# Optimization experiments

Hardware: AMD Instinct MI355X
Metric: run time of the kernel (lower is better)

Reference implementation:

```python
import jax, jax.numpy as jnp
import numpy as np

N, D, M, K = 65536, 128, 8, 256


def _quantize_stage(res, C):
    """Nearest-codeword lookup for one residual-quantizer stage.
    res: (N, D) residual vectors; C: (K, D) codebook.
    Returns (recon (N, D), one-hot code (N, K)).
    """
    # squared L2 distances via expansion: ||r||^2 - 2 r.C^T + ||c||^2
    d2 = (jnp.sum(res * res, axis=-1, keepdims=True)
          - 2.0 * jnp.einsum('nd,kd->nk', res, C)
          + jnp.sum(C * C, axis=-1))                      # (N, K)
    idx = jnp.argmin(d2, axis=-1)                          # (N,)
    onehot = jax.nn.one_hot(idx, K, dtype=res.dtype)       # (N, K)
    recon = jnp.einsum('nk,kd->nd', onehot, C)             # gather via one-hot matmul
    return recon, onehot


def setup_inputs() -> dict:
    key = jax.random.key(0)
    kx, kc = jax.random.split(key)
    x = jax.random.normal(kx, (N, D), dtype=jnp.float32)
    # learned codebooks: one (K, D) table per stage, kaiming-uniform-like scale
    bound = float(np.sqrt(6.0 / D))
    codebooks = jax.random.uniform(kc, (M, K, D), dtype=jnp.float32,
                                   minval=-bound, maxval=bound)
    return {"x": x, "codebooks": codebooks}


def reference(x, codebooks):
    # Sequential residual quantization: M stages, strict data dependency.
    x_recon, code0 = _quantize_stage(x, codebooks[0])
    codes = [code0[:, None, :]]          # (N, 1, K)
    side_output = [x_recon]
    res = x - x_recon
    for i in range(1, M):
        res_recon, code = _quantize_stage(res, codebooks[i])
        codes.append(code[:, None, :])
        x_recon = x_recon + res_recon
        side_output.append(x_recon)
        res = x - x_recon
    codes = jnp.concatenate(codes, axis=1)       # (N, M, K) one-hot
    side_output = jnp.stack(side_output, axis=0)  # (M, N, D)
    return (x_recon, codes, side_output)
```

## Files before the change

### kernel.cpp

```cpp
#include <hip/hip_runtime.h>


constexpr int NV = 65536;
constexpr int DD = 128;
constexpr int MS = 8;
constexpr int KC = 256;
constexpr int CH = 112;
constexpr int CST = 20;
constexpr int RST = 8 * CST;

template<int CTRL>
__device__ __forceinline__ float bfly_add(float v) {
    int p = __builtin_amdgcn_update_dpp(__float_as_int(v), __float_as_int(v),
                                        CTRL, 0xF, 0xF, true);
    return v + __int_as_float(p);
}

__global__ __launch_bounds__(256, 2)
void rq_kernel(const float* __restrict__ x,
               const float* __restrict__ cb,
               float* __restrict__ out)
{
    const int tid = threadIdx.x;
    const int c   = tid & 7;
    const int grp = tid >> 3;
    const size_t vbase = (size_t)blockIdx.x * 128 + (size_t)grp * 4;

    __shared__ __align__(16) float sC[CH * RST];
    __shared__ float cn_s[CH];

    float rA[4][16], cA[4][16];

    #pragma unroll
    for (int v = 0; v < 4; ++v) {
        const float* xr = x + (vbase + v) * DD + c;
        #pragma unroll
        for (int k = 0; k < 16; ++k) {
            rA[v][k] = xr[8 * k];
            cA[v][k] = 0.0f;
        }
    }

    float* out_recon = out;
    float* out_codes = out + (size_t)NV * DD;
    float* out_side  = out_codes + (size_t)NV * MS * KC;

    for (int m = 0; m < MS; ++m) {
        const float* C = cb + (size_t)m * KC * DD;

        float rn[4];
        #pragma unroll
        for (int v = 0; v < 4; ++v) {
            float p = rA[v][0] * rA[v][0];
            #pragma unroll
            for (int k = 1; k < 16; ++k) p += rA[v][k] * rA[v][k];
            p = bfly_add<0xB1>(p);
            p = bfly_add<0x4E>(p);
            p = bfly_add<0x141>(p);
            rn[v] = p;
        }

        float best[4]; int bi[4];
        #pragma unroll
        for (int v = 0; v < 4; ++v) { best[v] = 3.402823466e38f; bi[v] = 0; }

        for (int base = 0; base < KC; base += CH) {
            const int rows = (KC - base) < CH ? (KC - base) : CH;

            __syncthreads();

            {
                const float4* g4 = (const float4*)(C + (size_t)base * DD);
                const int nf4 = rows * 32;
                for (int i = tid; i < nf4; i += 256) {
                    float4 v = g4[i];
                    const int row = i >> 5;
                    const int j   = i & 31;
                    const int c0  = (j & 1) * 4;
                    const int k   = j >> 1;
                    float* dst = sC + row * RST + c0 * CST + k;
                    dst[0 * CST] = v.x;
                    dst[1 * CST] = v.y;
                    dst[2 * CST] = v.z;
                    dst[3 * CST] = v.w;
                }
            }
            if (tid < rows) {
                const float* cr = C + (size_t)(base + tid) * DD;
                float p[8];
                #pragma unroll
                for (int j = 0; j < 8; ++j) { float v = cr[j]; p[j] = v * v; }
                #pragma unroll
                for (int i = 8; i < DD; i += 8) {
                    #pragma unroll
                    for (int j = 0; j < 8; ++j) { float v = cr[i + j]; p[j] += v * v; }
                }
                cn_s[tid] = ((p[0]+p[1]) + (p[2]+p[3])) + ((p[4]+p[5]) + (p[6]+p[7]));
            }
            __syncthreads();

            #pragma unroll 2
            for (int kk = 0; kk < rows; ++kk) {
                const float4* cr4 = (const float4*)(sC + kk * RST + c * CST);
                float pa[4];
                {
                    float4 a = cr4[0];
                    #pragma unroll
                    for (int v = 0; v < 4; ++v) {
                        pa[v]  = rA[v][0] * a.x;
                        pa[v] += rA[v][1] * a.y;
                        pa[v] += rA[v][2] * a.z;
                        pa[v] += rA[v][3] * a.w;
                    }
                }
                #pragma unroll
                for (int t = 1; t < 4; ++t) {
                    float4 a = cr4[t];
                    #pragma unroll
                    for (int v = 0; v < 4; ++v) {
                        pa[v] += rA[v][4*t    ] * a.x;
                        pa[v] += rA[v][4*t + 1] * a.y;
                        pa[v] += rA[v][4*t + 2] * a.z;
                        pa[v] += rA[v][4*t + 3] * a.w;
                    }
                }
                const float cn = cn_s[kk];
                #pragma unroll
                for (int v = 0; v < 4; ++v) {
                    float s = pa[v];
                    s = bfly_add<0xB1>(s);
                    s = bfly_add<0x4E>(s);
                    s = bfly_add<0x141>(s);
                    float dist = (rn[v] - 2.0f * s) + cn;
                    if (dist < best[v]) { best[v] = dist; bi[v] = base + kk; }
                }
            }
        }

        #pragma unroll
        for (int v = 0; v < 4; ++v) {
            const size_t n = vbase + v;
            const float* cw = C + (size_t)bi[v] * DD + c;
            const float* xr = x + n * DD + c;
            float* so = out_side + ((size_t)m * NV + n) * DD + c;
            #pragma unroll
            for (int k = 0; k < 16; ++k) {
                float cv = cw[8 * k];
                float xv = xr[8 * k];
                cA[v][k] += cv;
                rA[v][k] = xv - cA[v][k];
                so[8 * k] = cA[v][k];
            }
        }

        #pragma unroll
        for (int v = 0; v < 4; ++v) {
            const size_t n = vbase + v;
            float* crow = out_codes + n * (size_t)(MS * KC) + (size_t)m * KC;
            const int b = bi[v];
            #pragma unroll
            for (int j4 = 0; j4 < 32; j4 += 4) {
                const int j = c * 32 + j4;
                float4 w;
                w.x = (b == j    ) ? 1.0f : 0.0f;
                w.y = (b == j + 1) ? 1.0f : 0.0f;
                w.z = (b == j + 2) ? 1.0f : 0.0f;
                w.w = (b == j + 3) ? 1.0f : 0.0f;
                *(float4*)(crow + j) = w;
            }
        }
    }

    #pragma unroll
    for (int v = 0; v < 4; ++v) {
        float* ro = out_recon + (vbase + v) * DD + c;
        #pragma unroll
        for (int k = 0; k < 16; ++k) ro[8 * k] = cA[v][k];
    }
}

extern "C" void kernel_launch(void* const* d_in, const int* in_sizes, int n_in,
                              void* d_out, int out_size, void* d_ws, size_t ws_size,
                              hipStream_t stream)
{
    const float* x  = (const float*)d_in[0];
    const float* cb = (const float*)d_in[1];
    float* out = (float*)d_out;
    rq_kernel<<<dim3(NV / 128), dim3(256), 0, stream>>>(x, cb, out);
}
```

Baseline: 1.617 ms.

## Split codeword search across two thread halves and merge argmin via LDS

The block grows to 512 threads. Each half scans a different half of the 256 codewords for the same 128 vectors, in three staged chunks that hold rows from both halves. The per-half best distance and index are merged through shared memory, and the output writes are divided so one half writes the side and reconstruction outputs while the other writes the one-hot codes. This doubles the threads working on the distance computation and removes the serial dependency over all K codewords per thread, at the cost of redundant residual updates in both halves, an extra reduction step, and higher register pressure under launch_bounds(512,4).

```diff
diff --git a/kernel.cpp b/kernel.cpp
--- a/kernel.cpp
+++ b/kernel.cpp
@@ -9,6 +9,10 @@
 constexpr int CST = 20;
 constexpr int RST = 8 * CST;
 
+constexpr int CB0[3]  = {0, 56, 112};
+constexpr int CB1[3]  = {128, 184, 240};
+constexpr int CCNT[3] = {56, 56, 16};
+
 template<int CTRL>
 __device__ __forceinline__ float bfly_add(float v) {
     int p = __builtin_amdgcn_update_dpp(__float_as_int(v), __float_as_int(v),
@@ -16,14 +20,15 @@
     return v + __int_as_float(p);
 }
 
-__global__ __launch_bounds__(256, 2)
+__global__ __launch_bounds__(512, 4)
 void rq_kernel(const float* __restrict__ x,
                const float* __restrict__ cb,
                float* __restrict__ out)
 {
     const int tid = threadIdx.x;
+    const int h   = tid >> 8;
     const int c   = tid & 7;
-    const int grp = tid >> 3;
+    const int grp = (tid >> 3) & 31;
     const size_t vbase = (size_t)blockIdx.x * 128 + (size_t)grp * 4;
 
     __shared__ __align__(16) float sC[CH * RST];
@@ -62,31 +67,36 @@
 
         float best[4]; int bi[4];
         #pragma unroll
-        for (int v = 0; v < 4; ++v) { best[v] = 3.402823466e38f; bi[v] = 0; }
-
-        for (int base = 0; base < KC; base += CH) {
-            const int rows = (KC - base) < CH ? (KC - base) : CH;
+        for (int v = 0; v < 4; ++v) { best[v] = 3.402823466e38f; bi[v] = h * 128; }
+
+        #pragma unroll
+        for (int ch = 0; ch < 3; ++ch) {
+            const int cnt = CCNT[ch];
 
             __syncthreads();
 
             {
-                const float4* g4 = (const float4*)(C + (size_t)base * DD);
-                const int nf4 = rows * 32;
-                for (int i = tid; i < nf4; i += 256) {
-                    float4 v = g4[i];
-                    const int row = i >> 5;
-                    const int j   = i & 31;
-                    const int c0  = (j & 1) * 4;
-                    const int k   = j >> 1;
-                    float* dst = sC + row * RST + c0 * CST + k;
+                const float4* g4 = (const float4*)C;
+                const int nf4 = 2 * cnt * 32;
+                for (int i = tid; i < nf4; i += 512) {
+                    const int slot = i >> 5;
+                    const int j    = i & 31;
+                    const int grow = (slot < cnt) ? (CB0[ch] + slot)
+                                                  : (CB1[ch] + slot - cnt);
+                    float4 v = g4[grow * 32 + j];
+                    const int c0 = (j & 1) * 4;
+                    const int k  = j >> 1;
+                    float* dst = sC + slot * RST + c0 * CST + k;
                     dst[0 * CST] = v.x;
                     dst[1 * CST] = v.y;
                     dst[2 * CST] = v.z;
                     dst[3 * CST] = v.w;
                 }
             }
-            if (tid < rows) {
-                const float* cr = C + (size_t)(base + tid) * DD;
+            if (tid < 2 * cnt) {
+                const int grow = (tid < cnt) ? (CB0[ch] + tid)
+                                             : (CB1[ch] + tid - cnt);
+                const float* cr = C + (size_t)grow * DD;
                 float p[8];
                 #pragma unroll
                 for (int j = 0; j < 8; ++j) { float v = cr[j]; p[j] = v * v; }
@@ -99,9 +109,12 @@
             }
             __syncthreads();
 
+            const int slot0 = h * cnt;
+            const int gbase = h ? CB1[ch] : CB0[ch];
+
             #pragma unroll 2
-            for (int kk = 0; kk < rows; ++kk) {
-                const float4* cr4 = (const float4*)(sC + kk * RST + c * CST);
+            for (int kk = 0; kk < cnt; ++kk) {
+                const float4* cr4 = (const float4*)(sC + (slot0 + kk) * RST + c * CST);
                 float pa[4];
                 {
                     float4 a = cr4[0];
@@ -124,7 +137,7 @@
                         pa[v] += rA[v][4*t + 3] * a.w;
                     }
                 }
-                const float cn = cn_s[kk];
+                const float cn = cn_s[slot0 + kk];
                 #pragma unroll
                 for (int v = 0; v < 4; ++v) {
                     float s = pa[v];
@@ -132,8 +145,31 @@
                     s = bfly_add<0x4E>(s);
                     s = bfly_add<0x141>(s);
                     float dist = (rn[v] - 2.0f * s) + cn;
-                    if (dist < best[v]) { best[v] = dist; bi[v] = base + kk; }
-                }
+                    if (dist < best[v]) { best[v] = dist; bi[v] = gbase + kk; }
+                }
+            }
+        }
+
+        __syncthreads();
+        {
+            float* mb = sC;
+            int*   mi = (int*)(sC + 2048);
+            #pragma unroll
+            for (int v = 0; v < 4; ++v) {
+                mb[v * 512 + tid] = best[v];
+                mi[v * 512 + tid] = bi[v];
+            }
+            __syncthreads();
+            const int ptid = tid ^ 256;
+            #pragma unroll
+            for (int v = 0; v < 4; ++v) {
+                const float pb = mb[v * 512 + ptid];
+                const int   pi = mi[v * 512 + ptid];
+                float lob, hib; int loi, hii;
+                if (h == 0) { lob = best[v]; loi = bi[v]; hib = pb;      hii = pi;    }
+                else        { lob = pb;      loi = pi;    hib = best[v]; hii = bi[v]; }
+                if (hib < lob) { best[v] = hib; bi[v] = hii; }
+                else           { best[v] = lob; bi[v] = loi; }
             }
         }
 
@@ -142,40 +178,47 @@
             const size_t n = vbase + v;
             const float* cw = C + (size_t)bi[v] * DD + c;
             const float* xr = x + n * DD + c;
-            float* so = out_side + ((size_t)m * NV + n) * DD + c;
             #pragma unroll
             for (int k = 0; k < 16; ++k) {
                 float cv = cw[8 * k];
                 float xv = xr[8 * k];
                 cA[v][k] += cv;
                 rA[v][k] = xv - cA[v][k];
-                so[8 * k] = cA[v][k];
-            }
-        }
-
+            }
+            if (h == 0) {
+                float* so = out_side + ((size_t)m * NV + n) * DD + c;
+                #pragma unroll
+                for (int k = 0; k < 16; ++k) so[8 * k] = cA[v][k];
+            }
+        }
+
+        if (h == 1) {
+            #pragma unroll
+            for (int v = 0; v < 4; ++v) {
+                const size_t n = vbase + v;
+                float* crow = out_codes + n * (size_t)(MS * KC) + (size_t)m * KC;
+                const int b = bi[v];
+                #pragma unroll
+                for (int j4 = 0; j4 < 32; j4 += 4) {
+                    const int j = c * 32 + j4;
+                    float4 w;
+                    w.x = (b == j    ) ? 1.0f : 0.0f;
+                    w.y = (b == j + 1) ? 1.0f : 0.0f;
+                    w.z = (b == j + 2) ? 1.0f : 0.0f;
+                    w.w = (b == j + 3) ? 1.0f : 0.0f;
+                    *(float4*)(crow + j) = w;
+                }
+            }
+        }
+    }
+
+    if (h == 0) {
         #pragma unroll
         for (int v = 0; v < 4; ++v) {
-            const size_t n = vbase + v;
-            float* crow = out_codes + n * (size_t)(MS * KC) + (size_t)m * KC;
-            const int b = bi[v];
-            #pragma unroll
-            for (int j4 = 0; j4 < 32; j4 += 4) {
-                const int j = c * 32 + j4;
-                float4 w;
-                w.x = (b == j    ) ? 1.0f : 0.0f;
-                w.y = (b == j + 1) ? 1.0f : 0.0f;
-                w.z = (b == j + 2) ? 1.0f : 0.0f;
-                w.w = (b == j + 3) ? 1.0f : 0.0f;
-                *(float4*)(crow + j) = w;
-            }
-        }
-    }
-
-    #pragma unroll
-    for (int v = 0; v < 4; ++v) {
-        float* ro = out_recon + (vbase + v) * DD + c;
-        #pragma unroll
-        for (int k = 0; k < 16; ++k) ro[8 * k] = cA[v][k];
+            float* ro = out_recon + (vbase + v) * DD + c;
+            #pragma unroll
+            for (int k = 0; k < 16; ++k) ro[8 * k] = cA[v][k];
+        }
     }
 }
 
@@ -186,5 +229,5 @@
     const float* x  = (const float*)d_in[0];
     const float* cb = (const float*)d_in[1];
     float* out = (float*)d_out;
-    rq_kernel<<<dim3(NV / 128), dim3(256), 0, stream>>>(x, cb, out);
+    rq_kernel<<<dim3(NV / 128), dim3(512), 0, stream>>>(x, cb, out);
 }
```

New measurement: 2.083 ms. 28.8% more time.
